# Kernel tuning notes

Hardware: AMD Instinct MI355X
Metric: run time of the kernel (lower is better)

Reference implementation:

```python
import jax, jax.numpy as jnp
import numpy as np

B, L, D, H, M = 4, 2048, 256, 8, 256
HEAD = D // H
EPS = 1e-6


def _pos_embedding(maxlen, d):
    i = np.arange(maxlen, dtype=np.float64)[:, None]
    j = np.arange(d, dtype=np.float64)[None, :]
    angle = i / np.power(10000.0, (j - (j % 2)) / d)
    pe = np.where(j % 2 == 0, np.sin(angle), np.cos(angle))
    return jnp.asarray(pe, jnp.float32)  # [L, D]


def _projection_matrix(m, d, seed=0):
    # FAVOR+ orthogonal random features: one full QR block (m == d here),
    # rows rescaled by norms of iid Gaussian rows (scaling=0 in source).
    rng = np.random.default_rng(seed)
    block = rng.standard_normal((d, d))
    q, _ = np.linalg.qr(block)
    q = q.T[:m]
    mult = np.linalg.norm(rng.standard_normal((m, d)), axis=1)
    return jnp.asarray(mult[:, None] * q, jnp.float32)  # [M, D]


def _softmax_kernel(x, is_query, proj):
    # x: [B, L, H, D], proj: [M, D]
    d = x.shape[-1]
    m = proj.shape[0]
    x = x * (float(d) ** -0.25)
    xp = jnp.einsum('blhd,md->blhm', x, proj)
    diag = 0.5 * jnp.sum(x * x, axis=-1, keepdims=True)
    if is_query:
        mx = jnp.max(xp, axis=-1, keepdims=True)
    else:
        mx = jnp.max(xp, axis=(-3, -1), keepdims=True)  # over L and M
    return (float(m) ** -0.5) * (jnp.exp(xp - diag - mx) + EPS)


def setup_inputs() -> dict:
    key = jax.random.key(0)
    ks = jax.random.split(key, 12)
    s = 1.0 / np.sqrt(D)
    inp = {
        'query': jax.random.normal(ks[0], (B, L, D), jnp.float32),
        'key': jax.random.normal(ks[1], (B, L, D), jnp.float32),
        'value': jax.random.normal(ks[2], (B, L, D), jnp.float32),
        'mask': jnp.ones((B, L), jnp.float32),
        'Wq': jax.random.normal(ks[3], (D, D), jnp.float32) * s,
        'bq': jnp.zeros((D,), jnp.float32),
        'Wk': jax.random.normal(ks[4], (D, D), jnp.float32) * s,
        'bk': jnp.zeros((D,), jnp.float32),
        'Wv': jax.random.normal(ks[5], (D, D), jnp.float32) * s,
        'bv': jnp.zeros((D,), jnp.float32),
        'Wo': jax.random.normal(ks[6], (D, D), jnp.float32) * s,
        'bo': jnp.zeros((D,), jnp.float32),
        'proj': _projection_matrix(M, D, seed=0),
        'pos': _pos_embedding(L, D),
    }
    return inp


def reference(query, key, value, mask, Wq, bq, Wk, bk, Wv, bv, Wo, bo, proj, pos):
    b = query.shape[0]
    q = query @ Wq + bq                      # [B, L, D]
    k = key @ Wk + bk
    v = value @ Wv + bv
    # per-head copies keep the FULL model_size feature dim (as in source)
    q = jnp.broadcast_to(q[:, :, None, :], (b, L, H, D))
    k = jnp.broadcast_to(k[:, :, None, :], (b, L, H, D))
    pos_b = pos[None]                        # [1, L, D]
    cos_pos = jnp.repeat(pos_b[..., None, 1::2], 2, axis=-1)  # [1, L, 1, D]
    sin_pos = jnp.repeat(pos_b[..., None, ::2], 2, axis=-1)

    def rot(x):
        x2 = jnp.stack([-x[..., 1::2], x[..., ::2]], axis=-1).reshape(x.shape)
        return x * cos_pos + x2 * sin_pos

    q = rot(q)
    k = rot(k)
    v = v.reshape(b, L, H, HEAD)

    qp = _softmax_kernel(q, True, proj)      # [B, L, H, M]
    kp = _softmax_kernel(k, False, proj)     # [B, L, H, M]

    kvs = jnp.einsum('blhm,blhd->bhmd', kp, v)
    num = jnp.einsum('blhm,bhmd->blhd', qp, kvs)
    den = jnp.einsum('blhm,bhm->blh', qp, jnp.sum(kp, axis=1))
    ctx = (num / den[..., None]).reshape(b, L, D)
    return ctx @ Wo + bo
```

## Files before the change

kernel.cpp:

```cpp
#include <hip/hip_runtime.h>

typedef unsigned short u16;
typedef unsigned int u32;
typedef __bf16 bf16x8 __attribute__((ext_vector_type(8)));
typedef float f32x4 __attribute__((ext_vector_type(4)));

__device__ __forceinline__ float bf2f(u16 u) { return __uint_as_float(((u32)u) << 16); }
__device__ __forceinline__ u16 f2bf(float f) {
  u32 x = __float_as_uint(f);
  x += 0x7fffu + ((x >> 16) & 1u);
  return (u16)(x >> 16);
}
__device__ __forceinline__ u32 encf(float x) {
  u32 u = __float_as_uint(x);
  return (u >> 31) ? ~u : (u | 0x80000000u);
}
__device__ __forceinline__ float decf(u32 e) {
  return (e >> 31) ? __uint_as_float(e & 0x7fffffffu) : __uint_as_float(~e);
}

#define MFMA(a, b, c) __builtin_amdgcn_mfma_f32_16x16x32_bf16(a, b, c, 0, 0, 0)

__global__ __launch_bounds__(256) void prep_w(
    const float* Wq, const float* Wk, const float* Wv, const float* Wo,
    const float* proj, const float* bv,
    u16* WqT, u16* WkT, u16* projb, u16* WWT, float* bw,
    float* __restrict__ ksum, u32* __restrict__ mxk) {
  __shared__ u16 tsh[32][33];
  __shared__ u16 As[64][40];
  __shared__ u16 Bs[64][40];
  const int z = blockIdx.z;
  const int x = threadIdx.x, y = threadIdx.y;
  const int tid = y * 32 + x;
  if (z < 2) {
    const float* s = z == 0 ? Wq : Wk;
    u16* d = z == 0 ? WqT : WkT;
    int r0 = blockIdx.y * 32, c0 = blockIdx.x * 32;
#pragma unroll
    for (int i = 0; i < 32; i += 8) tsh[y + i][x] = f2bf(s[(r0 + y + i) * 256 + c0 + x]);
    __syncthreads();
#pragma unroll
    for (int i = 0; i < 32; i += 8) d[(c0 + y + i) * 256 + r0 + x] = tsh[x][y + i];
    return;
  }
  if (z == 2) {
    int r0 = blockIdx.y * 32, c0 = blockIdx.x * 32;
#pragma unroll
    for (int i = 0; i < 32; i += 8)
      projb[(r0 + y + i) * 256 + c0 + x] = f2bf(proj[(r0 + y + i) * 256 + c0 + x]);
    return;
  }
  if (blockIdx.x < 4 && blockIdx.y < 4) {
    const int o0 = blockIdx.x * 64, i0 = blockIdx.y * 64;
    const int lane = tid & 63, wid = tid >> 6;
    const int wm = (wid >> 1) * 32, wn = (wid & 1) * 32;
    const int fm = lane & 15, fq = (lane >> 4) * 8, rowq = (lane >> 4) * 4;
    const int dr = tid >> 3, oc = (tid & 7) * 8;
    const int ir = tid >> 2, dc = (tid & 3) * 8;
    f32x4 acc[2][2] = {};
    for (int it = 0; it < 8; ++it) {
      int d0 = it * 32;
      float4 w0 = *(const float4*)(Wo + (d0 + dr) * 256 + o0 + oc);
      float4 w1 = *(const float4*)(Wo + (d0 + dr) * 256 + o0 + oc + 4);
      float4 v0 = *(const float4*)(Wv + (i0 + ir) * 256 + d0 + dc);
      float4 v1 = *(const float4*)(Wv + (i0 + ir) * 256 + d0 + dc + 4);
      __syncthreads();
      float wv[8] = {w0.x, w0.y, w0.z, w0.w, w1.x, w1.y, w1.z, w1.w};
#pragma unroll
      for (int j = 0; j < 8; ++j) As[oc + j][dr] = f2bf(wv[j]);
      u16* bp = &Bs[ir][dc];
      bp[0] = f2bf(v0.x); bp[1] = f2bf(v0.y); bp[2] = f2bf(v0.z); bp[3] = f2bf(v0.w);
      bp[4] = f2bf(v1.x); bp[5] = f2bf(v1.y); bp[6] = f2bf(v1.z); bp[7] = f2bf(v1.w);
      __syncthreads();
      bf16x8 a0 = *(const bf16x8*)&As[wm + fm][fq];
      bf16x8 a1 = *(const bf16x8*)&As[wm + 16 + fm][fq];
      bf16x8 b0 = *(const bf16x8*)&Bs[wn + fm][fq];
      bf16x8 b1 = *(const bf16x8*)&Bs[wn + 16 + fm][fq];
      acc[0][0] = MFMA(a0, b0, acc[0][0]);
      acc[0][1] = MFMA(a0, b1, acc[0][1]);
      acc[1][0] = MFMA(a1, b0, acc[1][0]);
      acc[1][1] = MFMA(a1, b1, acc[1][1]);
    }
#pragma unroll
    for (int mt = 0; mt < 2; ++mt)
#pragma unroll
      for (int nt = 0; nt < 2; ++nt)
#pragma unroll
        for (int r = 0; r < 4; ++r)
          WWT[(o0 + wm + mt * 16 + rowq + r) * 256 + i0 + wn + nt * 16 + fm] =
              f2bf(acc[mt][nt][r]);
    return;
  }
  if (blockIdx.x == 4 && blockIdx.y == 0) {
    float s = 0.0f;
    for (int d = 0; d < 256; ++d) s = fmaf(bv[d], Wo[d * 256 + tid], s);
    bw[tid] = s;
    for (int i = tid; i < 1024; i += 256) ksum[i] = 0.0f;
    if (tid < 4) mxk[tid] = 0u;
  }
}

__global__ __launch_bounds__(256, 3) void projrot2(
    const float* __restrict__ Xq, const float* __restrict__ Xk,
    const u16* __restrict__ WqT, const u16* __restrict__ WkT,
    const float* __restrict__ bq, const float* __restrict__ bk,
    const float* __restrict__ pos, const u16* __restrict__ projb,
    float* __restrict__ diag_k, u16* __restrict__ qp,
    float* __restrict__ xp, u32* __restrict__ mxk) {
  const int mode = blockIdx.z;
  const float* X = mode ? Xq : Xk;
  const u16* W = mode ? WqT : WkT;
  const float* bias = mode ? bq : bk;
  __shared__ u16 As[32][40];
  __shared__ u16 Bs[256][40];
  __shared__ u16 cbuf[32][264];
  __shared__ float dred[2][32];
  __shared__ float mred[2][32];
  __shared__ float wred[4];
  const int row0 = blockIdx.x * 32;
  const int t = threadIdx.x;
  const int lane = t & 63, wid = t >> 6;
  const int wrow = wid & 1, wcol = wid >> 1;
  const int fm = lane & 15, fq = (lane >> 4) * 8, rowq = (lane >> 4) * 4;
  const int ar = t >> 3, ak = (t & 7) * 4;

  f32x4 acc[8] = {};
  float4 av = *(const float4*)(X + (long long)(row0 + ar) * 256 + ak);
  uint4 bv0 = ((const uint4*)(W + (long long)t * 256))[0];
  uint4 bv1 = ((const uint4*)(W + (long long)t * 256))[1];
  uint4 bv2 = ((const uint4*)(W + (long long)t * 256))[2];
  uint4 bv3 = ((const uint4*)(W + (long long)t * 256))[3];
  for (int s = 0; s < 8; ++s) {
    __syncthreads();
    As[ar][ak] = f2bf(av.x); As[ar][ak + 1] = f2bf(av.y);
    As[ar][ak + 2] = f2bf(av.z); As[ar][ak + 3] = f2bf(av.w);
    uint4* bsp = (uint4*)&Bs[t][0];
    bsp[0] = bv0; bsp[1] = bv1; bsp[2] = bv2; bsp[3] = bv3;
    __syncthreads();
    if (s < 7) {
      const int k1 = (s + 1) * 32;
      av = *(const float4*)(X + (long long)(row0 + ar) * 256 + k1 + ak);
      const uint4* wn = (const uint4*)(W + (long long)t * 256 + k1);
      bv0 = wn[0]; bv1 = wn[1]; bv2 = wn[2]; bv3 = wn[3];
    }
    bf16x8 af = *(const bf16x8*)&As[wrow * 16 + fm][fq];
#pragma unroll
    for (int j = 0; j < 8; ++j) {
      bf16x8 bf = *(const bf16x8*)&Bs[wcol * 128 + j * 16 + fm][fq];
      acc[j] = MFMA(af, bf, acc[j]);
    }
  }

  float dsum[4] = {};
#pragma unroll
  for (int j = 0; j < 8; ++j) {
    float bb2 = bias[wcol * 128 + j * 16 + fm];
#pragma unroll
    for (int r = 0; r < 4; ++r) {
      float v = acc[j][r] + bb2;
      acc[j][r] = v;
      dsum[r] += v * v;
    }
  }
#pragma unroll
  for (int o = 1; o < 16; o <<= 1)
#pragma unroll
    for (int r = 0; r < 4; ++r) dsum[r] += __shfl_xor(dsum[r], o, 64);
  if (fm == 0) {
#pragma unroll
    for (int r = 0; r < 4; ++r) dred[wcol][wrow * 16 + rowq + r] = dsum[r];
  }
  __syncthreads();
  if (mode == 0 && t < 32) diag_k[row0 + t] = 0.03125f * (dred[0][t] + dred[1][t]);

#pragma unroll
  for (int j = 0; j < 8; ++j) {
    const int c = wcol * 128 + j * 16 + fm;
#pragma unroll
    for (int r = 0; r < 4; ++r) {
      const int row = wrow * 16 + rowq + r;
      const int l = (row0 + row) & 2047;
      float v = acc[j][r];
      float prt = __shfl_xor(v, 1, 64);
      float x2 = (fm & 1) ? prt : -prt;
      float2 cs = *(const float2*)(pos + (long long)l * 256 + (c & ~1));
      cbuf[row][c] = f2bf(0.25f * (v * cs.y + x2 * cs.x));
    }
  }

  f32x4 acc2[8] = {};
  uint4 pv0 = ((const uint4*)(projb + (long long)t * 256))[0];
  uint4 pv1 = ((const uint4*)(projb + (long long)t * 256))[1];
  uint4 pv2 = ((const uint4*)(projb + (long long)t * 256))[2];
  uint4 pv3 = ((const uint4*)(projb + (long long)t * 256))[3];
  for (int s = 0; s < 8; ++s) {
    __syncthreads();
    uint4* bsp = (uint4*)&Bs[t][0];
    bsp[0] = pv0; bsp[1] = pv1; bsp[2] = pv2; bsp[3] = pv3;
    __syncthreads();
    if (s < 7) {
      const uint4* pn = (const uint4*)(projb + (long long)t * 256 + (s + 1) * 32);
      pv0 = pn[0]; pv1 = pn[1]; pv2 = pn[2]; pv3 = pn[3];
    }
    bf16x8 af = *(const bf16x8*)&cbuf[wrow * 16 + fm][s * 32 + fq];
#pragma unroll
    for (int j = 0; j < 8; ++j) {
      bf16x8 bf = *(const bf16x8*)&Bs[wcol * 128 + j * 16 + fm][fq];
      acc2[j] = MFMA(af, bf, acc2[j]);
    }
  }

  if (mode == 1) {
    float m4[4] = {-3.0e38f, -3.0e38f, -3.0e38f, -3.0e38f};
#pragma unroll
    for (int j = 0; j < 8; ++j)
#pragma unroll
      for (int r = 0; r < 4; ++r) m4[r] = fmaxf(m4[r], acc2[j][r]);
#pragma unroll
    for (int o = 1; o < 16; o <<= 1)
#pragma unroll
      for (int r = 0; r < 4; ++r) m4[r] = fmaxf(m4[r], __shfl_xor(m4[r], o, 64));
    if (fm == 0) {
#pragma unroll
      for (int r = 0; r < 4; ++r) mred[wcol][wrow * 16 + rowq + r] = m4[r];
    }
    __syncthreads();
#pragma unroll
    for (int j = 0; j < 8; ++j) {
      const int col = wcol * 128 + j * 16 + fm;
#pragma unroll
      for (int r = 0; r < 4; ++r) {
        const int row = wrow * 16 + rowq + r;
        float mxr = fmaxf(mred[0][row], mred[1][row]);
        float dgr = 0.03125f * (dred[0][row] + dred[1][row]);
        float v = 0.0625f * (__expf(acc2[j][r] - dgr - mxr) + 1e-6f);
        qp[(long long)(row0 + row) * 256 + col] = f2bf(v);
      }
    }
  } else {
    float mx = -3.0e38f;
#pragma unroll
    for (int j = 0; j < 8; ++j) {
      int col = wcol * 128 + j * 16 + fm;
#pragma unroll
      for (int r = 0; r < 4; ++r) {
        float v = acc2[j][r];
        xp[(long long)(row0 + wrow * 16 + rowq + r) * 256 + col] = v;
        mx = fmaxf(mx, v);
      }
    }
#pragma unroll
    for (int o = 32; o > 0; o >>= 1) mx = fmaxf(mx, __shfl_xor(mx, o, 64));
    if (lane == 0) wred[wid] = mx;
    __syncthreads();
    if (t == 0) {
      float m = fmaxf(fmaxf(wred[0], wred[1]), fmaxf(wred[2], wred[3]));
      atomicMax(mxk + (row0 >> 11), encf(m));
    }
  }
}

__global__ __launch_bounds__(256) void kvs_raw_split(
    const float* __restrict__ xp, const float* __restrict__ Xv,
    const float* __restrict__ diag_k, const u32* __restrict__ mxk,
    float* __restrict__ part, float* __restrict__ ksum) {
  __shared__ union USM {
    struct { u16 As[64][40]; u16 Bs[64][40]; } s;
    float ksbuf[32][65];
  } sm;
  const int mxt = blockIdx.x, ny = blockIdx.y, z = blockIdx.z;
  const int b = z >> 2, kc = z & 3;
  const long long l0 = (long long)b * 2048 + kc * 512;
  const int t = threadIdx.x;
  const int lane = t & 63, wid = t >> 6;
  const int wrow = wid >> 1, wcol = wid & 1;
  const int fm = lane & 15, fq = (lane >> 4) * 8, rowq = (lane >> 4) * 4;
  const float mxv = decf(mxk[b]);
  const int sr = t >> 3, sc = (t & 7) * 8;
  f32x4 acc[2][2] = {};
  float ksp[8] = {};
  long long lrow = l0 + sr;
  float4 x0 = *(const float4*)(xp + lrow * 256 + mxt * 64 + sc);
  float4 x1 = *(const float4*)(xp + lrow * 256 + mxt * 64 + sc + 4);
  float4 v0 = *(const float4*)(Xv + lrow * 256 + ny * 64 + sc);
  float4 v1 = *(const float4*)(Xv + lrow * 256 + ny * 64 + sc + 4);
  float dgl = diag_k[lrow];
  for (int s = 0; s < 16; ++s) {
    float xv[8] = {x0.x, x0.y, x0.z, x0.w, x1.x, x1.y, x1.z, x1.w};
    float vv[8] = {v0.x, v0.y, v0.z, v0.w, v1.x, v1.y, v1.z, v1.w};
    u16 kpv[8], vpv[8];
#pragma unroll
    for (int j = 0; j < 8; ++j) {
      float v = 0.0625f * (__expf(xv[j] - dgl - mxv) + 1e-6f);
      kpv[j] = f2bf(v);
      ksp[j] += bf2f(kpv[j]);
      vpv[j] = f2bf(vv[j]);
    }
    __syncthreads();
#pragma unroll
    for (int j = 0; j < 8; ++j) {
      sm.s.As[sc + j][sr] = kpv[j];
      sm.s.Bs[sc + j][sr] = vpv[j];
    }
    __syncthreads();
    if (s < 15) {
      lrow = l0 + (s + 1) * 32 + sr;
      x0 = *(const float4*)(xp + lrow * 256 + mxt * 64 + sc);
      x1 = *(const float4*)(xp + lrow * 256 + mxt * 64 + sc + 4);
      v0 = *(const float4*)(Xv + lrow * 256 + ny * 64 + sc);
      v1 = *(const float4*)(Xv + lrow * 256 + ny * 64 + sc + 4);
      dgl = diag_k[lrow];
    }
    bf16x8 a0 = *(const bf16x8*)&sm.s.As[wrow * 32 + fm][fq];
    bf16x8 a1 = *(const bf16x8*)&sm.s.As[wrow * 32 + 16 + fm][fq];
    bf16x8 b0 = *(const bf16x8*)&sm.s.Bs[wcol * 32 + fm][fq];
    bf16x8 b1 = *(const bf16x8*)&sm.s.Bs[wcol * 32 + 16 + fm][fq];
    acc[0][0] = MFMA(a0, b0, acc[0][0]);
    acc[0][1] = MFMA(a0, b1, acc[0][1]);
    acc[1][0] = MFMA(a1, b0, acc[1][0]);
    acc[1][1] = MFMA(a1, b1, acc[1][1]);
  }
#pragma unroll
  for (int mt = 0; mt < 2; ++mt)
#pragma unroll
    for (int nt = 0; nt < 2; ++nt)
#pragma unroll
      for (int r = 0; r < 4; ++r)
        part[(long long)z * 65536 +
             (long long)(mxt * 64 + wrow * 32 + mt * 16 + rowq + r) * 256 +
             ny * 64 + wcol * 32 + nt * 16 + fm] = acc[mt][nt][r];
  __syncthreads();
#pragma unroll
  for (int j = 0; j < 8; ++j) sm.ksbuf[sr][sc + j] = ksp[j];
  __syncthreads();
  if (ny == 0 && t < 64) {
    float ssum = 0.0f;
    for (int r = 0; r < 32; ++r) ssum += sm.ksbuf[r][t];
    atomicAdd(ksum + b * 256 + mxt * 64 + t, ssum);
  }
}

__global__ __launch_bounds__(256) void kvsw(
    const u16* __restrict__ WWT, const float* __restrict__ part,
    const float* __restrict__ ksum, const float* __restrict__ bw,
    u16* __restrict__ kvsWT) {
  __shared__ u16 As[64][40];
  __shared__ u16 Bs[64][40];
  const int o0 = blockIdx.x * 64, m0 = blockIdx.y * 64, b = blockIdx.z;
  const int t = threadIdx.x;
  const int lane = t & 63, wid = t >> 6;
  const int wm = (wid >> 1) * 32, wn = (wid & 1) * 32;
  const int fm = lane & 15, fq = (lane >> 4) * 8, rowq = (lane >> 4) * 4;
  const int arow = t >> 2, acol = (t & 3) * 8;
  f32x4 acc[2][2] = {};
  for (int it = 0; it < 8; ++it) {
    int k0 = it * 32;
    uint4 av = *(const uint4*)(WWT + (o0 + arow) * 256 + k0 + acol);
    float4 s0 = {0, 0, 0, 0}, s1 = {0, 0, 0, 0};
#pragma unroll
    for (int kc = 0; kc < 4; ++kc) {
      const float* pp = part + (long long)(b * 4 + kc) * 65536 + (long long)(m0 + arow) * 256 + k0 + acol;
      float4 u0 = *(const float4*)(pp);
      float4 u1 = *(const float4*)(pp + 4);
      s0.x += u0.x; s0.y += u0.y; s0.z += u0.z; s0.w += u0.w;
      s1.x += u1.x; s1.y += u1.y; s1.z += u1.z; s1.w += u1.w;
    }
    __syncthreads();
    *(uint4*)&As[arow][acol] = av;
    u16* bp = &Bs[arow][acol];
    bp[0] = f2bf(s0.x); bp[1] = f2bf(s0.y); bp[2] = f2bf(s0.z); bp[3] = f2bf(s0.w);
    bp[4] = f2bf(s1.x); bp[5] = f2bf(s1.y); bp[6] = f2bf(s1.z); bp[7] = f2bf(s1.w);
    __syncthreads();
    bf16x8 a0 = *(const bf16x8*)&As[wm + fm][fq];
    bf16x8 a1 = *(const bf16x8*)&As[wm + 16 + fm][fq];
    bf16x8 b0 = *(const bf16x8*)&Bs[wn + fm][fq];
    bf16x8 b1 = *(const bf16x8*)&Bs[wn + 16 + fm][fq];
    acc[0][0] = MFMA(a0, b0, acc[0][0]);
    acc[0][1] = MFMA(a0, b1, acc[0][1]);
    acc[1][0] = MFMA(a1, b0, acc[1][0]);
    acc[1][1] = MFMA(a1, b1, acc[1][1]);
  }
#pragma unroll
  for (int mt = 0; mt < 2; ++mt)
#pragma unroll
    for (int nt = 0; nt < 2; ++nt) {
      int col = m0 + wn + nt * 16 + fm;
      float ksv = ksum[b * 256 + col];
#pragma unroll
      for (int r = 0; r < 4; ++r) {
        int row = o0 + wm + mt * 16 + rowq + r;
        float v = acc[mt][nt][r] + bw[row] * ksv;
        kvsWT[(long long)b * 65536 + (long long)row * 256 + col] = f2bf(v);
      }
    }
}

__global__ __launch_bounds__(256, 4) void numout(
    const u16* __restrict__ qp, const float* __restrict__ ksum,
    const u16* __restrict__ kvsWT, const float* __restrict__ bo,
    float* __restrict__ out) {
  __shared__ u16 As[16][40];
  __shared__ u16 Bs[256][40];
  __shared__ float ksm[256], dsh[16];
  const int row0 = blockIdx.x * 16;
  const int b = blockIdx.z;
  const long long qrow = (long long)b * 2048 + row0;
  const int t = threadIdx.x;
  const int lane = t & 63, wid = t >> 6;
  const int fm = lane & 15, fq = (lane >> 4) * 8, rowq = (lane >> 4) * 4;
  const int ar = t >> 4, ak = (t & 15) * 2;

  u32 a0 = *(const u32*)(qp + (qrow + ar) * 256 + ak);
  const u16* kvr = kvsWT + (long long)b * 65536 + (long long)t * 256;
  uint4 bv0 = ((const uint4*)kvr)[0];
  uint4 bv1 = ((const uint4*)kvr)[1];
  uint4 bv2 = ((const uint4*)kvr)[2];
  uint4 bv3 = ((const uint4*)kvr)[3];

  ksm[t] = ksum[b * 256 + t];
  const int prow = t >> 4, pc0 = (t & 15) * 16;
  const u16* qr = qp + (qrow + prow) * 256 + pc0;
  uint4 u0 = *(const uint4*)(qr);
  uint4 u1 = *(const uint4*)(qr + 8);
  __syncthreads();

  float denp = 0.0f;
  u32 uu[8] = {u0.x, u0.y, u0.z, u0.w, u1.x, u1.y, u1.z, u1.w};
#pragma unroll
  for (int j = 0; j < 8; ++j) {
    denp += bf2f((u16)(uu[j] & 0xffffu)) * ksm[pc0 + 2 * j];
    denp += bf2f((u16)(uu[j] >> 16)) * ksm[pc0 + 2 * j + 1];
  }
#pragma unroll
  for (int o = 1; o < 16; o <<= 1) denp += __shfl_xor(denp, o, 64);
  if ((t & 15) == 0) dsh[prow] = denp;

  f32x4 acc[4] = {};
  for (int s = 0; s < 8; ++s) {
    __syncthreads();
    *(u32*)&As[ar][ak] = a0;
    uint4* bsp = (uint4*)&Bs[t][0];
    bsp[0] = bv0; bsp[1] = bv1; bsp[2] = bv2; bsp[3] = bv3;
    __syncthreads();
    if (s < 7) {
      const int k1 = (s + 1) * 32;
      a0 = *(const u32*)(qp + (qrow + ar) * 256 + k1 + ak);
      const uint4* kn = (const uint4*)(kvr + k1);
      bv0 = kn[0]; bv1 = kn[1]; bv2 = kn[2]; bv3 = kn[3];
    }
    bf16x8 af = *(const bf16x8*)&As[fm][fq];
#pragma unroll
    for (int j = 0; j < 4; ++j) {
      bf16x8 bf = *(const bf16x8*)&Bs[wid * 64 + j * 16 + fm][fq];
      acc[j] = MFMA(af, bf, acc[j]);
    }
  }
#pragma unroll
  for (int j = 0; j < 4; ++j) {
    int col = wid * 64 + j * 16 + fm;
    float bb2 = bo[col];
#pragma unroll
    for (int r = 0; r < 4; ++r) {
      int l = rowq + r;
      out[(qrow + l) * 256 + col] = acc[j][r] / dsh[l] + bb2;
    }
  }
}

extern "C" void kernel_launch(void* const* d_in, const int* in_sizes, int n_in,
                              void* d_out, int out_size, void* d_ws, size_t ws_size,
                              hipStream_t stream) {
  (void)in_sizes; (void)n_in; (void)out_size; (void)ws_size;
  const float* query = (const float*)d_in[0];
  const float* key = (const float*)d_in[1];
  const float* value = (const float*)d_in[2];
  const float* Wq = (const float*)d_in[4];
  const float* bq = (const float*)d_in[5];
  const float* Wk = (const float*)d_in[6];
  const float* bk = (const float*)d_in[7];
  const float* Wv = (const float*)d_in[8];
  const float* bv = (const float*)d_in[9];
  const float* Wo = (const float*)d_in[10];
  const float* bo = (const float*)d_in[11];
  const float* proj = (const float*)d_in[12];
  const float* pos = (const float*)d_in[13];

  char* w = (char*)d_ws;
  u16* qp = (u16*)(w);
  float* xp = (float*)(w + (8 << 20));
  float* part = (float*)(w + (16 << 20));
  u16* kvsWT = (u16*)(w + (20 << 20));
  u16* WqT = (u16*)(w + (21 << 20));
  u16* WkT = WqT + 65536;
  u16* projb = WkT + 65536;
  u16* WWT = projb + 65536;
  float* diag_k = (float*)(w + (22 << 20));
  float* ksum = diag_k + 8192;
  float* bw = ksum + 1024;
  u32* mxk = (u32*)(bw + 256);

  prep_w<<<dim3(8, 8, 4), dim3(32, 8), 0, stream>>>(Wq, Wk, Wv, Wo, proj, bv,
                                                    WqT, WkT, projb, WWT, bw,
                                                    ksum, mxk);
  projrot2<<<dim3(256, 1, 2), dim3(256), 0, stream>>>(
      query, key, WqT, WkT, bq, bk, pos, projb, diag_k, qp, xp, mxk);
  kvs_raw_split<<<dim3(4, 4, 16), dim3(256), 0, stream>>>(xp, value, diag_k, mxk,
                                                          part, ksum);
  kvsw<<<dim3(4, 4, 4), dim3(256), 0, stream>>>(WWT, part, ksum, bw, kvsWT);
  numout<<<dim3(128, 1, 4), dim3(256), 0, stream>>>(qp, ksum, kvsWT, bo,
                                                    (float*)d_out);
}
```

Before: 81.12 us.

## Double L-split in kvs kernel and retile kvsw into more smaller blocks

```diff
diff --git a/kernel.cpp b/kernel.cpp
--- a/kernel.cpp
+++ b/kernel.cpp
@@ -260,7 +260,7 @@
   }
 }
 
-__global__ __launch_bounds__(256) void kvs_raw_split(
+__global__ __launch_bounds__(256, 2) void kvs_raw_split(
     const float* __restrict__ xp, const float* __restrict__ Xv,
     const float* __restrict__ diag_k, const u32* __restrict__ mxk,
     float* __restrict__ part, float* __restrict__ ksum) {
@@ -269,8 +269,8 @@
     float ksbuf[32][65];
   } sm;
   const int mxt = blockIdx.x, ny = blockIdx.y, z = blockIdx.z;
-  const int b = z >> 2, kc = z & 3;
-  const long long l0 = (long long)b * 2048 + kc * 512;
+  const int b = z >> 3, kc = z & 7;
+  const long long l0 = (long long)b * 2048 + kc * 256;
   const int t = threadIdx.x;
   const int lane = t & 63, wid = t >> 6;
   const int wrow = wid >> 1, wcol = wid & 1;
@@ -285,7 +285,7 @@
   float4 v0 = *(const float4*)(Xv + lrow * 256 + ny * 64 + sc);
   float4 v1 = *(const float4*)(Xv + lrow * 256 + ny * 64 + sc + 4);
   float dgl = diag_k[lrow];
-  for (int s = 0; s < 16; ++s) {
+  for (int s = 0; s < 8; ++s) {
     float xv[8] = {x0.x, x0.y, x0.z, x0.w, x1.x, x1.y, x1.z, x1.w};
     float vv[8] = {v0.x, v0.y, v0.z, v0.w, v1.x, v1.y, v1.z, v1.w};
     u16 kpv[8], vpv[8];
@@ -303,7 +303,7 @@
       sm.s.Bs[sc + j][sr] = vpv[j];
     }
     __syncthreads();
-    if (s < 15) {
+    if (s < 7) {
       lrow = l0 + (s + 1) * 32 + sr;
       x0 = *(const float4*)(xp + lrow * 256 + mxt * 64 + sc);
       x1 = *(const float4*)(xp + lrow * 256 + mxt * 64 + sc + 4);
@@ -345,54 +345,52 @@
     const float* __restrict__ ksum, const float* __restrict__ bw,
     u16* __restrict__ kvsWT) {
   __shared__ u16 As[64][40];
-  __shared__ u16 Bs[64][40];
-  const int o0 = blockIdx.x * 64, m0 = blockIdx.y * 64, b = blockIdx.z;
+  __shared__ u16 Bs[16][40];
+  const int bid = blockIdx.x;
+  const int b = bid >> 6;
+  const int o0 = ((bid >> 4) & 3) * 64;
+  const int m0 = (bid & 15) * 16;
   const int t = threadIdx.x;
-  const int lane = t & 63, wid = t >> 6;
-  const int wm = (wid >> 1) * 32, wn = (wid & 1) * 32;
+  const int w4 = t >> 6;
+  const int lane = t & 63;
   const int fm = lane & 15, fq = (lane >> 4) * 8, rowq = (lane >> 4) * 4;
   const int arow = t >> 2, acol = (t & 3) * 8;
-  f32x4 acc[2][2] = {};
-  for (int it = 0; it < 8; ++it) {
-    int k0 = it * 32;
-    uint4 av = *(const uint4*)(WWT + (o0 + arow) * 256 + k0 + acol);
-    float4 s0 = {0, 0, 0, 0}, s1 = {0, 0, 0, 0};
-#pragma unroll
-    for (int kc = 0; kc < 4; ++kc) {
-      const float* pp = part + (long long)(b * 4 + kc) * 65536 + (long long)(m0 + arow) * 256 + k0 + acol;
-      float4 u0 = *(const float4*)(pp);
-      float4 u1 = *(const float4*)(pp + 4);
-      s0.x += u0.x; s0.y += u0.y; s0.z += u0.z; s0.w += u0.w;
-      s1.x += u1.x; s1.y += u1.y; s1.z += u1.z; s1.w += u1.w;
-    }
+  const int brow = t >> 4, bcol = (t & 15) * 2;
+  f32x4 acc = {0.0f, 0.0f, 0.0f, 0.0f};
+  uint4 av = *(const uint4*)(WWT + (o0 + arow) * 256 + acol);
+  float2 ps[8];
+  {
+    const float* pb = part + (long long)(b * 8) * 65536 + (m0 + brow) * 256 + bcol;
+#pragma unroll
+    for (int kc = 0; kc < 8; ++kc) ps[kc] = *(const float2*)(pb + (long long)kc * 65536);
+  }
+  for (int s = 0; s < 8; ++s) {
+    float sx = ps[0].x + ps[1].x + ps[2].x + ps[3].x + ps[4].x + ps[5].x + ps[6].x + ps[7].x;
+    float sy = ps[0].y + ps[1].y + ps[2].y + ps[3].y + ps[4].y + ps[5].y + ps[6].y + ps[7].y;
     __syncthreads();
     *(uint4*)&As[arow][acol] = av;
-    u16* bp = &Bs[arow][acol];
-    bp[0] = f2bf(s0.x); bp[1] = f2bf(s0.y); bp[2] = f2bf(s0.z); bp[3] = f2bf(s0.w);
-    bp[4] = f2bf(s1.x); bp[5] = f2bf(s1.y); bp[6] = f2bf(s1.z); bp[7] = f2bf(s1.w);
-    __syncthreads();
-    bf16x8 a0 = *(const bf16x8*)&As[wm + fm][fq];
-    bf16x8 a1 = *(const bf16x8*)&As[wm + 16 + fm][fq];
-    bf16x8 b0 = *(const bf16x8*)&Bs[wn + fm][fq];
-    bf16x8 b1 = *(const bf16x8*)&Bs[wn + 16 + fm][fq];
-    acc[0][0] = MFMA(a0, b0, acc[0][0]);
-    acc[0][1] = MFMA(a0, b1, acc[0][1]);
-    acc[1][0] = MFMA(a1, b0, acc[1][0]);
-    acc[1][1] = MFMA(a1, b1, acc[1][1]);
-  }
-#pragma unroll
-  for (int mt = 0; mt < 2; ++mt)
-#pragma unroll
-    for (int nt = 0; nt < 2; ++nt) {
-      int col = m0 + wn + nt * 16 + fm;
-      float ksv = ksum[b * 256 + col];
-#pragma unroll
-      for (int r = 0; r < 4; ++r) {
-        int row = o0 + wm + mt * 16 + rowq + r;
-        float v = acc[mt][nt][r] + bw[row] * ksv;
-        kvsWT[(long long)b * 65536 + (long long)row * 256 + col] = f2bf(v);
-      }
-    }
+    Bs[brow][bcol] = f2bf(sx);
+    Bs[brow][bcol + 1] = f2bf(sy);
+    __syncthreads();
+    if (s < 7) {
+      const int k1 = (s + 1) * 32;
+      av = *(const uint4*)(WWT + (o0 + arow) * 256 + k1 + acol);
+      const float* pb = part + (long long)(b * 8) * 65536 + (m0 + brow) * 256 + k1 + bcol;
+#pragma unroll
+      for (int kc = 0; kc < 8; ++kc) ps[kc] = *(const float2*)(pb + (long long)kc * 65536);
+    }
+    bf16x8 af = *(const bf16x8*)&As[w4 * 16 + fm][fq];
+    bf16x8 bf = *(const bf16x8*)&Bs[fm][fq];
+    acc = MFMA(af, bf, acc);
+  }
+  const int col = m0 + fm;
+  float ksv = ksum[b * 256 + col];
+#pragma unroll
+  for (int r = 0; r < 4; ++r) {
+    int row = o0 + w4 * 16 + rowq + r;
+    kvsWT[(long long)b * 65536 + (long long)row * 256 + col] =
+        f2bf(acc[r] + bw[row] * ksv);
+  }
 }
 
 __global__ __launch_bounds__(256, 4) void numout(
@@ -487,8 +485,8 @@
 
   char* w = (char*)d_ws;
   u16* qp = (u16*)(w);
-  float* xp = (float*)(w + (8 << 20));
-  float* part = (float*)(w + (16 << 20));
+  float* xp = (float*)(w + (4 << 20));
+  float* part = (float*)(w + (12 << 20));
   u16* kvsWT = (u16*)(w + (20 << 20));
   u16* WqT = (u16*)(w + (21 << 20));
   u16* WkT = WqT + 65536;
@@ -504,9 +502,9 @@
                                                     ksum, mxk);
   projrot2<<<dim3(256, 1, 2), dim3(256), 0, stream>>>(
       query, key, WqT, WkT, bq, bk, pos, projb, diag_k, qp, xp, mxk);
-  kvs_raw_split<<<dim3(4, 4, 16), dim3(256), 0, stream>>>(xp, value, diag_k, mxk,
+  kvs_raw_split<<<dim3(4, 4, 32), dim3(256), 0, stream>>>(xp, value, diag_k, mxk,
                                                           part, ksum);
-  kvsw<<<dim3(4, 4, 4), dim3(256), 0, stream>>>(WWT, part, ksum, bw, kvsWT);
+  kvsw<<<dim3(256), dim3(256), 0, stream>>>(WWT, part, ksum, bw, kvsWT);
   numout<<<dim3(128, 1, 4), dim3(256), 0, stream>>>(qp, ksum, kvsWT, bo,
                                                     (float*)d_out);
 }
```

After: 76.16 us. 6.1% less time.
